# Kernel tuning notes

Hardware: AMD Instinct MI355X
Metric: run time of the kernel (lower is better)

The kernel has to match this reference:

```python
import jax, jax.numpy as jnp
import numpy as np

N = 50000      # num nodes (== num segments for aggregation)
E = 800000     # num edges
D_IN = 128
D_OUT = 128


def setup_inputs() -> dict:
    key = jax.random.key(0)
    k1, k2, k3, k4, k5, k6 = jax.random.split(key, 6)
    x = jax.random.normal(k1, (N, D_IN), dtype=jnp.float32)
    edge_rows = jax.random.randint(k2, (E,), 0, N, dtype=jnp.int32)
    edge_cols = jax.random.randint(k3, (E,), 0, N, dtype=jnp.int32)
    edge_vals = jax.random.uniform(k4, (E,), dtype=jnp.float32)
    stdv = 1.0 / np.sqrt(D_OUT)
    weight = jax.random.uniform(k5, (D_IN, D_OUT), dtype=jnp.float32, minval=-stdv, maxval=stdv)
    root_weight = jax.random.uniform(k6, (D_IN, D_OUT), dtype=jnp.float32, minval=-stdv, maxval=stdv)
    return {"x": x, "edge_rows": edge_rows, "edge_cols": edge_cols,
            "edge_vals": edge_vals, "weight": weight, "root_weight": root_weight}


def reference(x, edge_rows, edge_cols, edge_vals, weight, root_weight):
    # support = x @ W                                  [N, D_OUT]
    support = jnp.dot(x, weight)
    # out = spmm(adj, support): adj in COO form.
    # message per edge: adj[r, c] * support[c]         [E, D_OUT]
    msgs = support[edge_cols] * edge_vals[:, None]
    agg = jax.ops.segment_sum(msgs, edge_rows, num_segments=N)  # [N, D_OUT]
    # out += x @ W_root  (bias=False configuration)
    return agg + jnp.dot(x, root_weight)
```

## Files before the change

### kernel.cpp

```cpp
#include <hip/hip_runtime.h>

#define D 128
#define NCK 512
#define RPB 32
#define CHUNKCAP 1600
#define BCAP 1024
#define SCANW 2048
#define RAWB 29184

typedef short short8 __attribute__((ext_vector_type(8)));
typedef float v4f __attribute__((ext_vector_type(4)));
typedef float float2v __attribute__((ext_vector_type(2)));

static __device__ __forceinline__ unsigned short f2bf(float f) {
    unsigned u = __builtin_bit_cast(unsigned, f);
    u = (u + 0x7FFFu + ((u >> 16) & 1u)) >> 16;
    return (unsigned short)u;
}

__global__ __launch_bounds__(256) void wt_prep(
    const float* __restrict__ W, const float* __restrict__ Wr,
    unsigned short* __restrict__ Wt)
{
    const int gid = (int)blockIdx.x * 256 + (int)threadIdx.x;
    const int k  = gid >> 8;
    const int nn = gid & 255;
    const float v = (nn < D) ? W[k * D + nn] : Wr[k * D + (nn - D)];
    Wt[nn * D + k] = f2bf(v);
}

__global__ __launch_bounds__(256) void prep_gemm(
    const int* __restrict__ rows, const int* __restrict__ cols,
    const float* __restrict__ vals,
    unsigned* __restrict__ pkT, int2* __restrict__ sortedB,
    const float* __restrict__ x, const unsigned short* __restrict__ Wt,
    unsigned short* __restrict__ support, unsigned short* __restrict__ rootbuf,
    int M, int E, int nbuck, int chunk)
{
    __shared__ __align__(16) char raw[RAWB];
    __shared__ int wsumK[4];
    const int t = threadIdx.x;
    const int lane = t & 63, w = t >> 6;

    if ((int)blockIdx.x < NCK) {
        int* hist = (int*)raw;
        int* cur  = hist + SCANW;
        int2* stg = (int2*)(raw + 2 * SCANW * 4);
        const int c = blockIdx.x;

        #pragma unroll
        for (int j = 0; j < SCANW / 256; ++j) hist[t + j * 256] = 0;
        __syncthreads();

        const int base = c * chunk;
        const int endv = min(base + chunk, E);
        for (int e = base + t; e < endv; e += 256)
            atomicAdd(&hist[rows[e] >> 5], 1);
        __syncthreads();

        int lv[8];
        int ssum = 0;
        #pragma unroll
        for (int j = 0; j < 8; ++j) { lv[j] = hist[8 * t + j]; ssum += lv[j]; }
        int s = ssum;
        #pragma unroll
        for (int d = 1; d < 64; d <<= 1) {
            const int u = __shfl_up(s, d);
            if (lane >= d) s += u;
        }
        if (lane == 63) wsumK[w] = s;
        __syncthreads();
        int woff = 0;
        #pragma unroll
        for (int j = 0; j < 4; ++j) if (j < w) woff += wsumK[j];
        int run = woff + s - ssum;
        #pragma unroll
        for (int j = 0; j < 8; ++j) {
            const int idx = 8 * t + j;
            cur[idx] = run;
            if (idx < nbuck)
                pkT[(size_t)c * nbuck + idx] =
                    ((unsigned)lv[j] << 16) | (unsigned)run;
            run += lv[j];
        }
        __syncthreads();

        for (int e = base + t; e < endv; e += 256) {
            const int r  = rows[e];
            const int cc = cols[e];
            const float v = vals[e];
            const int pos = atomicAdd(&cur[r >> 5], 1);
            stg[pos] = make_int2(((r & (RPB - 1)) << 16) | cc, __float_as_int(v));
        }
        __syncthreads();

        const int n = endv - base;
        for (int k = t; k < n; k += 256)
            sortedB[(size_t)base + k] = stg[k];
        return;
    }

    unsigned short (*As)[136] = (unsigned short (*)[136])raw;
    const int nl = lane & 15, quad = lane >> 4;
    const int rowBase = ((int)blockIdx.x - NCK) * 64;

    {
        const int r = t & 63;
        const int seg = t >> 6;
        const int row = rowBase + r;
        unsigned short tmp[32];
        if (row < M) {
            const float4* src = (const float4*)(x + (size_t)row * D + seg * 32);
            #pragma unroll
            for (int j = 0; j < 8; ++j) {
                const float4 v = src[j];
                tmp[j * 4 + 0] = f2bf(v.x); tmp[j * 4 + 1] = f2bf(v.y);
                tmp[j * 4 + 2] = f2bf(v.z); tmp[j * 4 + 3] = f2bf(v.w);
            }
        } else {
            #pragma unroll
            for (int j = 0; j < 32; ++j) tmp[j] = 0;
        }
        #pragma unroll
        for (int j = 0; j < 4; ++j)
            *(short8*)&As[r][seg * 32 + j * 8] = *(const short8*)&tmp[j * 8];
    }

    short8 bfrag[4][4];
    {
        const unsigned short* wbase = Wt + (size_t)(w * 64 + nl) * D + quad * 8;
        #pragma unroll
        for (int nt = 0; nt < 4; ++nt)
            #pragma unroll
            for (int c = 0; c < 4; ++c)
                bfrag[c][nt] = *(const short8*)(wbase + (size_t)nt * 16 * D + c * 32);
    }
    __syncthreads();

    v4f acc[4][4] = {};
    #pragma unroll
    for (int c = 0; c < 4; ++c) {
        short8 afr[4];
        #pragma unroll
        for (int mt = 0; mt < 4; ++mt)
            afr[mt] = *(const short8*)&As[mt * 16 + nl][c * 32 + quad * 8];
        #pragma unroll
        for (int mt = 0; mt < 4; ++mt)
            #pragma unroll
            for (int nt = 0; nt < 4; ++nt)
                acc[mt][nt] = __builtin_amdgcn_mfma_f32_16x16x32_bf16(
                    afr[mt], bfrag[c][nt], acc[mt][nt], 0, 0, 0);
    }

    const int cbase = (w & 1) * 64;
    unsigned short* dst = (w < 2) ? support : rootbuf;
    #pragma unroll
    for (int mt = 0; mt < 4; ++mt)
        #pragma unroll
        for (int reg = 0; reg < 4; ++reg) {
            const int row = rowBase + mt * 16 + quad * 4 + reg;
            if (row < M) {
                #pragma unroll
                for (int nt = 0; nt < 4; ++nt)
                    dst[(size_t)row * D + cbase + nt * 16 + nl] = f2bf(acc[mt][nt][reg]);
            }
        }
}

__global__ __launch_bounds__(256) void transpose_pk(
    const unsigned* __restrict__ pkT, unsigned* __restrict__ pkTt, int nbuck)
{
    __shared__ unsigned tile[64][65];
    const int cb = (int)blockIdx.x & 7;
    const int bb = (int)blockIdx.x >> 3;
    const int t = threadIdx.x;
    for (int i = t; i < 64 * 64; i += 256) {
        const int lc = i & 63, lr = i >> 6;
        const int b = bb * 64 + lc, c = cb * 64 + lr;
        tile[lr][lc] = (b < nbuck) ? pkT[(size_t)c * nbuck + b] : 0u;
    }
    __syncthreads();
    for (int i = t; i < 64 * 64; i += 256) {
        const int lc = i & 63, lr = i >> 6;
        const int b = bb * 64 + lr, c = cb * 64 + lc;
        if (b < nbuck) pkTt[(size_t)b * NCK + c] = tile[lc][lr];
    }
}

__global__ __launch_bounds__(256) void sort_aggregate(
    const unsigned* __restrict__ pkTt, const int2* __restrict__ sortedB,
    const unsigned short* __restrict__ support,
    const unsigned short* __restrict__ rootbuf,
    float* __restrict__ out, int M, int nbuck, int chunk)
{
    __shared__ int2 stage[BCAP];
    __shared__ unsigned rowList[BCAP];
    __shared__ int wsum[4];
    __shared__ int rh[RPB];
    __shared__ int rs[RPB + 1];
    __shared__ int rcur[RPB];
    const int b = blockIdx.x, t = threadIdx.x;
    const int lane = t & 63, w = t >> 6;

    const uint2 pk2 = *(const uint2*)(pkTt + (size_t)b * NCK + 2 * t);
    const int cnt0 = (int)(pk2.x >> 16), off0 = (int)(pk2.x & 0xFFFFu);
    const int cnt1 = (int)(pk2.y >> 16), off1 = (int)(pk2.y & 0xFFFFu);
    int s = cnt0 + cnt1;
    #pragma unroll
    for (int d = 1; d < 64; d <<= 1) {
        const int u = __shfl_up(s, d);
        if (lane >= d) s += u;
    }
    if (lane == 63) wsum[w] = s;
    __syncthreads();
    int woff = 0, tot = 0;
    #pragma unroll
    for (int j = 0; j < 4; ++j) { const int v = wsum[j]; if (j < w) woff += v; tot += v; }
    const int incl = woff + s;
    const int base1 = incl - cnt1;
    const int base0 = base1 - cnt0;
    {
        const int2* src = sortedB + (size_t)(2 * t) * chunk + off0;
        int lim = min(base0 + cnt0, BCAP) - base0; if (lim < 0) lim = 0;
        for (int k = 0; k < lim; ++k) stage[base0 + k] = src[k];
    }
    {
        const int2* src = sortedB + (size_t)(2 * t + 1) * chunk + off1;
        int lim = min(base1 + cnt1, BCAP) - base1; if (lim < 0) lim = 0;
        for (int k = 0; k < lim; ++k) stage[base1 + k] = src[k];
    }
    if (t < RPB) rh[t] = 0;
    __syncthreads();

    const int T = min(tot, BCAP);
    for (int e = t; e < T; e += 256) atomicAdd(&rh[stage[e].x >> 16], 1);
    __syncthreads();
    if (t < 64) {
        const int mine = (t < RPB) ? rh[t] : 0;
        int v = mine;
        #pragma unroll
        for (int d = 1; d < RPB; d <<= 1) {
            const int u = __shfl_up(v, d);
            if (lane >= d) v += u;
        }
        if (t < RPB) {
            rs[t] = v - mine; rcur[t] = v - mine;
            if (t == RPB - 1) rs[RPB] = v;
        }
    }
    __syncthreads();
    for (int e = t; e < T; e += 256) {
        const int2 ed = stage[e];
        const int rib = ed.x >> 16;
        const int pos = atomicAdd(&rcur[rib], 1);
        rowList[pos] = ((unsigned)f2bf(__int_as_float(ed.y)) << 16)
                     | (unsigned)(ed.x & 0xFFFF);
    }
    __syncthreads();

    for (int r = w; r < RPB; r += 4) {
        const int row = b * RPB + r;
        if (row >= M) continue;
        const int st = rs[r], e2 = rs[r + 1];
        float ax = 0.f, ay = 0.f;
        int i = st;

        for (; i + 16 <= e2; i += 16) {
            unsigned d[16];
            #pragma unroll
            for (int j = 0; j < 16; ++j) d[j] = rowList[i + j];
            unsigned p[16];
            #pragma unroll
            for (int j = 0; j < 16; ++j)
                p[j] = *(const unsigned*)(support + (size_t)(d[j] & 0xFFFF) * D + lane * 2);
            #pragma unroll
            for (int j = 0; j < 16; ++j) {
                const float v = __builtin_bit_cast(float, d[j] & 0xFFFF0000u);
                ax += __builtin_bit_cast(float, p[j] << 16) * v;
                ay += __builtin_bit_cast(float, p[j] & 0xFFFF0000u) * v;
            }
        }
        if (i + 8 <= e2) {
            unsigned d[8];
            #pragma unroll
            for (int j = 0; j < 8; ++j) d[j] = rowList[i + j];
            unsigned p[8];
            #pragma unroll
            for (int j = 0; j < 8; ++j)
                p[j] = *(const unsigned*)(support + (size_t)(d[j] & 0xFFFF) * D + lane * 2);
            #pragma unroll
            for (int j = 0; j < 8; ++j) {
                const float v = __builtin_bit_cast(float, d[j] & 0xFFFF0000u);
                ax += __builtin_bit_cast(float, p[j] << 16) * v;
                ay += __builtin_bit_cast(float, p[j] & 0xFFFF0000u) * v;
            }
            i += 8;
        }
        if (i < e2) {
            const int m = e2 - i;
            unsigned d[8];
            #pragma unroll
            for (int j = 0; j < 8; ++j) {
                const int idx = i + (j < m ? j : m - 1);
                const unsigned q = rowList[idx];
                d[j] = (j < m) ? q : (q & 0xFFFFu);
            }
            unsigned p[8];
            #pragma unroll
            for (int j = 0; j < 8; ++j)
                p[j] = *(const unsigned*)(support + (size_t)(d[j] & 0xFFFF) * D + lane * 2);
            #pragma unroll
            for (int j = 0; j < 8; ++j) {
                const float v = __builtin_bit_cast(float, d[j] & 0xFFFF0000u);
                ax += __builtin_bit_cast(float, p[j] << 16) * v;
                ay += __builtin_bit_cast(float, p[j] & 0xFFFF0000u) * v;
            }
        }

        const unsigned pr = *(const unsigned*)(rootbuf + (size_t)row * D + lane * 2);
        float2v ov;
        ov.x = ax + __builtin_bit_cast(float, pr << 16);
        ov.y = ay + __builtin_bit_cast(float, pr & 0xFFFF0000u);
        __builtin_nontemporal_store(ov, (float2v*)(out + (size_t)row * D + lane * 2));
    }
}

extern "C" void kernel_launch(void* const* d_in, const int* in_sizes, int n_in,
                              void* d_out, int out_size, void* d_ws, size_t ws_size,
                              hipStream_t stream) {
    const float* x     = (const float*)d_in[0];
    const int*   erows = (const int*)d_in[1];
    const int*   ecols = (const int*)d_in[2];
    const float* evals = (const float*)d_in[3];
    const float* W     = (const float*)d_in[4];
    const float* Wr    = (const float*)d_in[5];
    float* out = (float*)d_out;

    const int M = in_sizes[0] / D;
    const int E = in_sizes[1];

    const int nbuck = (M + RPB - 1) / RPB;
    const int chunk = (E + NCK - 1) / NCK;
    const int nGemm = (M + 63) / 64;

    unsigned short* support = (unsigned short*)d_ws;
    unsigned short* rootbuf = support + (size_t)M * D;
    unsigned short* Wt      = rootbuf + (size_t)M * D;
    unsigned* pkT   = (unsigned*)(Wt + 2 * D * D);
    unsigned* pkTt  = pkT + (size_t)NCK * nbuck;
    int2*  sortedB  = (int2*)(pkTt + (size_t)nbuck * NCK);

    const int nTb = (nbuck + 63) / 64;

    wt_prep<<<128, 256, 0, stream>>>(W, Wr, Wt);
    prep_gemm<<<NCK + nGemm, 256, 0, stream>>>(
        erows, ecols, evals, pkT, sortedB, x, Wt, support, rootbuf,
        M, E, nbuck, chunk);
    transpose_pk<<<8 * nTb, 256, 0, stream>>>(pkT, pkTt, nbuck);
    sort_aggregate<<<nbuck, 256, 0, stream>>>(pkTt, sortedB,
                                              support, rootbuf, out, M, nbuck, chunk);
}
```

Baseline: 153.1 us.

## Split row gather into column quarters with four edges per wavefront step

The per-row aggregation loop now splits the 128 output columns into four 32-column quarters. In each pass, a wavefront's 64 lanes cover 4 edges times 16 column pairs, and the partial sums are reduced with cross-lane xor shuffles. This shrinks the working set touched in the support table during each pass, which may improve cache locality. In exchange it reads rowList four times, adds shuffle reductions and a block barrier per quarter, and drops the deep 16-wide load unrolling that gave memory-level parallelism.

```diff
diff --git a/kernel.cpp b/kernel.cpp
--- a/kernel.cpp
+++ b/kernel.cpp
@@ -258,70 +258,45 @@
     }
     __syncthreads();
 
-    for (int r = w; r < RPB; r += 4) {
-        const int row = b * RPB + r;
-        if (row >= M) continue;
-        const int st = rs[r], e2 = rs[r + 1];
-        float ax = 0.f, ay = 0.f;
-        int i = st;
-
-        for (; i + 16 <= e2; i += 16) {
-            unsigned d[16];
-            #pragma unroll
-            for (int j = 0; j < 16; ++j) d[j] = rowList[i + j];
-            unsigned p[16];
-            #pragma unroll
-            for (int j = 0; j < 16; ++j)
-                p[j] = *(const unsigned*)(support + (size_t)(d[j] & 0xFFFF) * D + lane * 2);
-            #pragma unroll
-            for (int j = 0; j < 16; ++j) {
-                const float v = __builtin_bit_cast(float, d[j] & 0xFFFF0000u);
-                ax += __builtin_bit_cast(float, p[j] << 16) * v;
-                ay += __builtin_bit_cast(float, p[j] & 0xFFFF0000u) * v;
+    const int eg = lane >> 4;
+    const int cp = lane & 15;
+    for (int q = 0; q < 4; ++q) {
+        const int qoff = q * 32 + cp * 2;
+        for (int r = w; r < RPB; r += 4) {
+            const int row = b * RPB + r;
+            if (row >= M) continue;
+            const int st = rs[r], e2 = rs[r + 1];
+            float ax = 0.f, ay = 0.f;
+            for (int i = st; i < e2; i += 8) {
+                #pragma unroll
+                for (int h = 0; h < 2; ++h) {
+                    const int ib = i + h * 4;
+                    if (ib < e2) {
+                        const int m = e2 - ib;
+                        const int idx = ib + (eg < m ? eg : m - 1);
+                        const unsigned ed = rowList[idx];
+                        const float v = (eg < m)
+                            ? __builtin_bit_cast(float, ed & 0xFFFF0000u) : 0.f;
+                        const unsigned p = *(const unsigned*)(
+                            support + (size_t)(ed & 0xFFFFu) * D + qoff);
+                        ax += __builtin_bit_cast(float, p << 16) * v;
+                        ay += __builtin_bit_cast(float, p & 0xFFFF0000u) * v;
+                    }
+                }
             }
-        }
-        if (i + 8 <= e2) {
-            unsigned d[8];
-            #pragma unroll
-            for (int j = 0; j < 8; ++j) d[j] = rowList[i + j];
-            unsigned p[8];
-            #pragma unroll
-            for (int j = 0; j < 8; ++j)
-                p[j] = *(const unsigned*)(support + (size_t)(d[j] & 0xFFFF) * D + lane * 2);
-            #pragma unroll
-            for (int j = 0; j < 8; ++j) {
-                const float v = __builtin_bit_cast(float, d[j] & 0xFFFF0000u);
-                ax += __builtin_bit_cast(float, p[j] << 16) * v;
-                ay += __builtin_bit_cast(float, p[j] & 0xFFFF0000u) * v;
+            ax += __shfl_xor(ax, 16); ay += __shfl_xor(ay, 16);
+            ax += __shfl_xor(ax, 32); ay += __shfl_xor(ay, 32);
+            if (eg == 0) {
+                const unsigned pr = *(const unsigned*)(
+                    rootbuf + (size_t)row * D + qoff);
+                float2v ov;
+                ov.x = ax + __builtin_bit_cast(float, pr << 16);
+                ov.y = ay + __builtin_bit_cast(float, pr & 0xFFFF0000u);
+                __builtin_nontemporal_store(ov,
+                    (float2v*)(out + (size_t)row * D + qoff));
             }
-            i += 8;
-        }
-        if (i < e2) {
-            const int m = e2 - i;
-            unsigned d[8];
-            #pragma unroll
-            for (int j = 0; j < 8; ++j) {
-                const int idx = i + (j < m ? j : m - 1);
-                const unsigned q = rowList[idx];
-                d[j] = (j < m) ? q : (q & 0xFFFFu);
-            }
-            unsigned p[8];
-            #pragma unroll
-            for (int j = 0; j < 8; ++j)
-                p[j] = *(const unsigned*)(support + (size_t)(d[j] & 0xFFFF) * D + lane * 2);
-            #pragma unroll
-            for (int j = 0; j < 8; ++j) {
-                const float v = __builtin_bit_cast(float, d[j] & 0xFFFF0000u);
-                ax += __builtin_bit_cast(float, p[j] << 16) * v;
-                ay += __builtin_bit_cast(float, p[j] & 0xFFFF0000u) * v;
-            }
-        }
-
-        const unsigned pr = *(const unsigned*)(rootbuf + (size_t)row * D + lane * 2);
-        float2v ov;
-        ov.x = ax + __builtin_bit_cast(float, pr << 16);
-        ov.y = ay + __builtin_bit_cast(float, pr & 0xFFFF0000u);
-        __builtin_nontemporal_store(ov, (float2v*)(out + (size_t)row * D + lane * 2));
+        }
+        __syncthreads();
     }
 }
 
```

After: 206.1 us. 1.35x slower.
